# Kernel tuning notes

Hardware: AMD Instinct MI355X
Metric: run time of the kernel (lower is better)

The kernel has to match this reference:

```python
import jax, jax.numpy as jnp
import numpy as np

NAMES = ['tempo', 'chord', 'barbeat', 'type', 'pitch', 'duration', 'velocity']
VOCABS = [56, 135, 18, 4, 87, 18, 25]
EMBS = [128, 256, 64, 32, 512, 128, 128]
B, S, D, H, L, FF = 2, 2048, 512, 8, 8, 2048
HD = D // H
EPS = 1e-6


def _layernorm(x, g, b):
    m = x.mean(-1, keepdims=True)
    v = ((x - m) ** 2).mean(-1, keepdims=True)
    return (x - m) / jnp.sqrt(v + 1e-5) * g + b


def _rope(x, cos, sin):
    x1, x2 = jnp.split(x, 2, -1)
    return x * cos + jnp.concatenate([-x2, x1], -1) * sin


def _causal_linear_attn(q, k, v):
    # kernelized causal linear attention: phi = elu + 1, cumulative-sum normalization
    q = jax.nn.elu(q) + 1.0
    k = jax.nn.elu(k) + 1.0
    kv = jnp.cumsum(jnp.einsum('bshd,bshm->bshdm', k, v), axis=1)  # [B,S,H,HD,HD]
    z = 1.0 / (jnp.einsum('bshd,bshd->bsh', q, jnp.cumsum(k, axis=1)) + EPS)
    return jnp.einsum('bshd,bshdm->bshm', q, kv) * z[..., None]


def _forward(inputs, target, emb_tables, in_W, in_b, Wq, bq, Wk, bk, Wv, bv, Wo, bo,
             ln1_g, ln1_b, ln2_g, ln2_b, W1, b1, W2, b2, norm_g, norm_b, pWs, pbs, catW, catb):
    # multi-field embedding, each scaled by sqrt(d_emb) (CPEmbedding)
    embs = [emb_tables[i][inputs[..., i]] * jnp.sqrt(jnp.float32(EMBS[i])) for i in range(7)]
    x = jnp.concatenate(embs, -1) @ in_W + in_b  # [B,S,D]
    # PositionalEncoding: original indexes pe at position seq_len -> single d_model vector
    div = jnp.exp(jnp.arange(0, D, 2, dtype=jnp.float32) * (-np.log(10000.0) / D))
    pe = jnp.zeros((D,), jnp.float32).at[0::2].set(jnp.sin(S * div)).at[1::2].set(jnp.cos(S * div))
    x = x + pe
    # rotary tables for head_dim
    inv_freq = 1.0 / (10000.0 ** (jnp.arange(0, HD, 2, dtype=jnp.float32) / HD))
    fr = jnp.arange(S, dtype=jnp.float32)[:, None] * inv_freq[None, :]
    ang = jnp.concatenate([fr, fr], -1)  # [S,HD]
    cos = jnp.cos(ang)[None, :, None, :]
    sin = jnp.sin(ang)[None, :, None, :]
    for l in range(L):
        q = (x @ Wq[l] + bq[l]).reshape(B, S, H, HD)
        k = (x @ Wk[l] + bk[l]).reshape(B, S, H, HD)
        v = (x @ Wv[l] + bv[l]).reshape(B, S, H, HD)
        q = _rope(q, cos, sin)
        k = _rope(k, cos, sin)
        a = _causal_linear_attn(q, k, v).reshape(B, S, D) @ Wo[l] + bo[l]
        x = x + a
        y = x = _layernorm(x, ln1_g[l], ln1_b[l])
        y = jax.nn.gelu(y @ W1[l] + b1[l], approximate=False) @ W2[l] + b2[l]
        x = _layernorm(x + y, ln2_g[l], ln2_b[l])
    x = _layernorm(x, norm_g, norm_b)
    # MultiProj with teacher-forced type embedding (target branch)
    emb_t = emb_tables[3][target[..., 3]] * jnp.sqrt(jnp.float32(EMBS[3]))
    proj_type = (x @ pWs[3] + pbs[3]) * jnp.sqrt(jnp.float32(VOCABS[3]))  # from pre-concat x
    xc = jnp.concatenate([x, emb_t], -1) @ catW + catb
    outs = []
    for i in range(7):
        if i == 3:
            outs.append(proj_type)
        else:
            outs.append((xc @ pWs[i] + pbs[i]) * jnp.sqrt(jnp.float32(VOCABS[i])))
    return jnp.concatenate(outs, -1)  # [B,S,sum(VOCABS)=343]


def setup_inputs():
    key = jax.random.key(0)
    kit = iter(jax.random.split(key, 64))
    s = 0.02
    d = {}
    d['inputs'] = jax.random.randint(next(kit), (B, S, 7), 0, 4)
    d['target'] = jax.random.randint(next(kit), (B, S, 7), 0, 4)
    for i, n in enumerate(NAMES):
        d['emb_' + n] = jax.random.normal(next(kit), (VOCABS[i], EMBS[i]), jnp.float32) * s
    E = sum(EMBS)
    d['in_W'] = jax.random.normal(next(kit), (E, D)) * s
    d['in_b'] = jnp.zeros((D,))
    for nm, sh in [('Wq', (L, D, D)), ('Wk', (L, D, D)), ('Wv', (L, D, D)), ('Wo', (L, D, D)), ('W1', (L, D, FF)), ('W2', (L, FF, D))]:
        d[nm] = jax.random.normal(next(kit), sh) * s
    for nm, sh in [('bq', (L, D)), ('bk', (L, D)), ('bv', (L, D)), ('bo', (L, D)), ('b1', (L, FF)), ('b2', (L, D)), ('ln1_b', (L, D)), ('ln2_b', (L, D)), ('norm_b', (D,)), ('catb', (D,))]:
        d[nm] = jnp.zeros(sh)
    d['ln1_g'] = jnp.ones((L, D))
    d['ln2_g'] = jnp.ones((L, D))
    d['norm_g'] = jnp.ones((D,))
    for i, n in enumerate(NAMES):
        d['pW_' + n] = jax.random.normal(next(kit), (D, VOCABS[i])) * s
        d['pb_' + n] = jnp.zeros((VOCABS[i],))
    d['catW'] = jax.random.normal(next(kit), (D + 32, D)) * s
    return d


def reference(inputs, target, emb_tempo, emb_chord, emb_barbeat, emb_type, emb_pitch, emb_duration, emb_velocity,
              in_W, in_b, Wq, bq, Wk, bk, Wv, bv, Wo, bo, ln1_g, ln1_b, ln2_g, ln2_b, W1, b1, W2, b2,
              norm_g, norm_b, pW_tempo, pb_tempo, pW_chord, pb_chord, pW_barbeat, pb_barbeat, pW_type, pb_type,
              pW_pitch, pb_pitch, pW_duration, pb_duration, pW_velocity, pb_velocity, catW, catb):
    emb_tables = [emb_tempo, emb_chord, emb_barbeat, emb_type, emb_pitch, emb_duration, emb_velocity]
    pWs = [pW_tempo, pW_chord, pW_barbeat, pW_type, pW_pitch, pW_duration, pW_velocity]
    pbs = [pb_tempo, pb_chord, pb_barbeat, pb_type, pb_pitch, pb_duration, pb_velocity]
    return _forward(inputs, target, emb_tables, in_W, in_b, Wq, bq, Wk, bk, Wv, bv, Wo, bo,
                    ln1_g, ln1_b, ln2_g, ln2_b, W1, b1, W2, b2, norm_g, norm_b, pWs, pbs, catW, catb)
```

## Files before the change

kernel.cpp:

```cpp
#include <hip/hip_runtime.h>
#include <math.h>

typedef unsigned short u16;
typedef short bf16x8 __attribute__((ext_vector_type(8)));
typedef float f32x4 __attribute__((ext_vector_type(4)));
typedef u16 u16x4 __attribute__((ext_vector_type(4)));
typedef u16 u16x8 __attribute__((ext_vector_type(8)));

#define NB 2
#define NS 2048
#define ND 512
#define NH 8
#define NHD 64
#define NL 8
#define NFF 2048
#define NM (NB*NS)
#define NE 1248
#define NEP 1280
#define NXC 576
#define CHK 64
#define NCH (NS/CHK)
#define QKVW 1536

__device__ inline float b2f(u16 u){ union{ unsigned int i; float f;} x; x.i = ((unsigned int)u)<<16; return x.f; }
__device__ inline u16 f2b(float f){ union{ float f; unsigned int i;} x; x.f=f; unsigned int r = x.i + 0x7fffu + ((x.i>>16)&1u); return (u16)(r>>16); }

__global__ void k_tables(float* rc, float* rs, float* pe){
  int tid = blockIdx.x*blockDim.x + threadIdx.x;
  if (tid < NS*32){
    int s = tid >> 5, j = tid & 31;
    double inv = exp(-(double)(2*j) * log(10000.0) / (double)NHD);
    double ang = (double)s * inv;
    rc[tid] = (float)cos(ang);
    rs[tid] = (float)sin(ang);
  }
  if (tid < ND/2){
    double div = exp(-(double)(2*tid) * log(10000.0) / (double)ND);
    double ang = (double)NS * div;
    pe[2*tid]   = (float)sin(ang);
    pe[2*tid+1] = (float)cos(ang);
  }
}

__global__ void k_embed(const int* __restrict__ inp,
    const float* __restrict__ e0, const float* __restrict__ e1, const float* __restrict__ e2,
    const float* __restrict__ e3, const float* __restrict__ e4, const float* __restrict__ e5,
    const float* __restrict__ e6, u16* __restrict__ xe)
{
  int row = blockIdx.x;
  int i0 = inp[row*7+0], i1 = inp[row*7+1], i2 = inp[row*7+2], i3 = inp[row*7+3],
      i4 = inp[row*7+4], i5 = inp[row*7+5], i6 = inp[row*7+6];
  size_t base = (size_t)row*NEP;
  for (int c = threadIdx.x; c < NEP; c += 256){
    float val = 0.f;
    if      (c < 128)  val = e0[i0*128 + c]        * 11.3137084990f;
    else if (c < 384)  val = e1[i1*256 + (c-128)]  * 16.0f;
    else if (c < 448)  val = e2[i2*64  + (c-384)]  * 8.0f;
    else if (c < 480)  val = e3[i3*32  + (c-448)]  * 5.6568542495f;
    else if (c < 992)  val = e4[i4*512 + (c-480)]  * 22.6274169980f;
    else if (c < 1120) val = e5[i5*128 + (c-992)]  * 11.3137084990f;
    else if (c < NE)   val = e6[i6*128 + (c-1120)] * 11.3137084990f;
    xe[base + c] = f2b(val);
  }
}

__device__ inline void trans_tile(const float* __restrict__ W, u16* __restrict__ WT,
                                  int K, int N, int Kpad, int bx, int by){
  __shared__ float t[32][33];
  int tx = threadIdx.x & 31, ty = threadIdx.x >> 5;
  int k0 = by*32, n0 = bx*32;
  #pragma unroll
  for (int i=0;i<4;i++){
    int k = k0 + ty + i*8, n = n0 + tx;
    t[ty+i*8][tx] = (k<K && n<N) ? W[(size_t)k*N + n] : 0.f;
  }
  __syncthreads();
  #pragma unroll
  for (int i=0;i<4;i++){
    int n = n0 + ty + i*8, k = k0 + tx;
    if (n<N && k<Kpad) WT[(size_t)n*Kpad + k] = f2b(t[tx][ty+i*8]);
  }
}
__global__ void k_trans(const float* __restrict__ W, u16* __restrict__ WT, int K, int N, int Kpad){
  trans_tile(W, WT, K, N, Kpad, blockIdx.x, blockIdx.y);
}
__global__ void k_trans4(const float* __restrict__ Wq, const float* __restrict__ Wk,
                         const float* __restrict__ Wv, const float* __restrict__ Wo,
                         u16* __restrict__ dst){
  int z = blockIdx.z, l = z>>2, s = z&3;
  const float* W = (s==0?Wq:s==1?Wk:s==2?Wv:Wo) + (size_t)l*ND*ND;
  trans_tile(W, dst + (size_t)z*ND*ND, ND, ND, ND, blockIdx.x, blockIdx.y);
}
__global__ void k_transw(const float* __restrict__ W1l, const float* __restrict__ W2l,
                         u16* __restrict__ w1T, u16* __restrict__ w2T){
  int bid = blockIdx.x;
  if (bid < 1024) trans_tile(W1l, w1T, ND, NFF, ND, bid & 63, bid >> 6);
  else { bid -= 1024; trans_tile(W2l, w2T, NFF, ND, NFF, bid & 15, bid >> 4); }
}

template<int ACT, int NT, int TM>
__global__ __launch_bounds__(256) void k_gemm(
    const u16* __restrict__ A, const u16* __restrict__ BT,
    const float* __restrict__ bias, float* __restrict__ Cf, u16* __restrict__ Cb,
    int N, int klen, int lda, int ldb, int ldc,
    int koff, float* __restrict__ Cf2,
    const float* __restrict__ rc, const float* __restrict__ rs)
{
  constexpr int MREP = TM/32;
  __shared__ u16 As[TM*64];
  __shared__ u16 Bs[NT*32*64];
  int tid = threadIdx.x;
  int w = tid >> 6, lane = tid & 63;

  int kz = blockIdx.z;
  A  += (size_t)kz*koff;
  BT += (size_t)kz*koff;
  if (kz){ Cf = Cf2; bias = nullptr; }

  int nwg = gridDim.x*gridDim.y;
  int d = blockIdx.y*gridDim.x + blockIdx.x;
  int wl = ((nwg & 7) == 0) ? ((d & 7)*(nwg >> 3) + (d >> 3)) : d;
  int bx = wl % gridDim.x, by = wl / gridDim.x;
  int m0 = by*TM, n0 = bx*(NT*32);

  f32x4 acc[MREP][NT];
  #pragma unroll
  for (int m=0;m<MREP;m++)
    #pragma unroll
    for (int n=0;n<NT;n++) acc[m][n] = (f32x4){0.f,0.f,0.f,0.f};

  int lg = lane>>3;
  int cg = (lane&7) ^ lg;
  const u16* ag = A  + (size_t)(m0 + w*(TM/4) + lg)*lda + cg*8;
  const u16* bg = BT + (size_t)(n0 + w*(NT*8) + lg)*ldb + cg*8;
  int wr = (w>>1)*(TM/2), wc = (w&1)*(NT*16);
  int lr = lane & 15;
  int rx = lr & 7;
  int cb_ = lane >> 4;
  int g = lane >> 4;

  int nk = klen >> 6;
  for (int t = 0; t < nk; ++t){
    int k0 = t << 6;
    #pragma unroll
    for (int i=0;i<TM/32;i++)
      __builtin_amdgcn_global_load_lds(
        (__attribute__((address_space(1))) void*)(void*)(ag + (size_t)(i*8)*lda + k0),
        (__attribute__((address_space(3))) void*)(&As[(w*(TM/4) + i*8)*64]), 16, 0, 0);
    #pragma unroll
    for (int j=0;j<NT;j++)
      __builtin_amdgcn_global_load_lds(
        (__attribute__((address_space(1))) void*)(void*)(bg + (size_t)(j*8)*ldb + k0),
        (__attribute__((address_space(3))) void*)(&Bs[(w*(NT*8) + j*8)*64]), 16, 0, 0);
    __syncthreads();
    #pragma unroll
    for (int kk=0;kk<2;kk++){
      int gA = ((kk*4 + cb_) ^ rx) * 8;
      bf16x8 af[MREP], bfr[NT];
      #pragma unroll
      for (int m=0;m<MREP;m++) af[m]  = *(const bf16x8*)&As[(wr + m*16 + lr)*64 + gA];
      #pragma unroll
      for (int n=0;n<NT;n++)   bfr[n] = *(const bf16x8*)&Bs[(wc + n*16 + lr)*64 + gA];
      #pragma unroll
      for (int m=0;m<MREP;m++)
        #pragma unroll
        for (int n=0;n<NT;n++)
          acc[m][n] = __builtin_amdgcn_mfma_f32_16x16x32_bf16(af[m], bfr[n], acc[m][n], 0,0,0);
    }
    __syncthreads();
  }

  if (ACT == 2){
    int colb = n0 + wc;
    if (colb < 1024){
      #pragma unroll
      for (int n=0;n<2;n++){
        int j = n*16 + lr;
        float bv1 = bias ? bias[colb+j]    : 0.f;
        float bv2 = bias ? bias[colb+j+32] : 0.f;
        #pragma unroll
        for (int m=0;m<MREP;m++){
          #pragma unroll
          for (int r=0;r<4;r++){
            int row = m0 + wr + m*16 + g*4 + r;
            int s = row & (NS-1);
            float c = rc[s*32+j], sn = rs[s*32+j];
            float a1 = acc[m][n][r]   + bv1;
            float a2 = acc[m][n+2][r] + bv2;
            float r1 = a1*c - a2*sn, r2 = a2*c + a1*sn;
            Cb[(size_t)row*ldc + colb + j]      = f2b((r1 > 0.f) ? r1+1.f : expf(r1));
            Cb[(size_t)row*ldc + colb + j + 32] = f2b((r2 > 0.f) ? r2+1.f : expf(r2));
          }
        }
      }
    } else {
      #pragma unroll
      for (int n=0;n<NT;n++){
        int col = colb + n*16 + lr;
        float bv = bias ? bias[col] : 0.f;
        #pragma unroll
        for (int m=0;m<MREP;m++)
          #pragma unroll
          for (int r=0;r<4;r++){
            int row = m0 + wr + m*16 + g*4 + r;
            Cb[(size_t)row*ldc + col] = f2b(acc[m][n][r] + bv);
          }
      }
    }
    return;
  }

  #pragma unroll
  for (int n=0;n<NT;n++){
    int col = n0 + wc + n*16 + lr;
    if (col < N){
      float bv = bias ? bias[col] : 0.f;
      #pragma unroll
      for (int m=0;m<MREP;m++){
        #pragma unroll
        for (int r=0;r<4;r++){
          int row = m0 + wr + m*16 + g*4 + r;
          float v = acc[m][n][r] + bv;
          if (ACT==1) v = 0.5f*v*(1.f+erff(v*0.70710678118654752f));
          if (Cf) Cf[(size_t)row*ldc + col] = v;
          if (Cb) Cb[(size_t)row*ldc + col] = f2b(v);
        }
      }
    }
  }
}

__global__ __launch_bounds__(256) void k_att1(const u16* __restrict__ qkv, float* __restrict__ pref){
  int c = blockIdx.x, h = blockIdx.y, b = blockIdx.z;
  __shared__ u16 Kt[64*64];
  __shared__ u16 Vt[80*64];
  int tid = threadIdx.x;
  {
    int t = tid & 63, dseg = (tid>>6)*16;
    const u16* kg = qkv + ((size_t)(b*NS + c*CHK + t))*QKVW + 512 + h*NHD + dseg;
    u16x8 k0 = *(const u16x8*)kg;
    u16x8 k1 = *(const u16x8*)(kg+8);
    u16x8 v0 = *(const u16x8*)(kg+512);
    u16x8 v1 = *(const u16x8*)(kg+520);
    #pragma unroll
    for (int e=0;e<8;e++){
      int d0 = dseg+e, d1 = dseg+8+e;
      Kt[(d0*64+t) ^ ((d0&7)<<3)] = k0[e];
      Kt[(d1*64+t) ^ ((d1&7)<<3)] = k1[e];
      Vt[(d0*64+t) ^ ((d0&7)<<3)] = v0[e];
      Vt[(d1*64+t) ^ ((d1&7)<<3)] = v1[e];
    }
    if (tid < 64) Vt[4096 + tid] = 0x3F80;
    for (int e = tid; e < 15*64; e += 256){
      int r = 65 + (e>>6), tt = e&63;
      Vt[(r*64+tt) ^ ((r&7)<<3)] = 0;
    }
  }
  __syncthreads();
  int lane = tid & 63, w = tid >> 6;
  int lr = lane & 15, lk = (lane>>4)*8;
  f32x4 acc[5];
  #pragma unroll
  for (int i=0;i<5;i++) acc[i] = (f32x4){0.f,0.f,0.f,0.f};
  #pragma unroll
  for (int kk=0;kk<2;kk++){
    int mcol = w*16 + lr;
    bf16x8 bfrag = *(const bf16x8*)&Kt[(mcol*64 + kk*32 + lk) ^ ((mcol&7)<<3)];
    #pragma unroll
    for (int fr=0; fr<5; fr++){
      int arow = fr*16 + lr;
      bf16x8 afrag = *(const bf16x8*)&Vt[(arow*64 + kk*32 + lk) ^ ((arow&7)<<3)];
      acc[fr] = __builtin_amdgcn_mfma_f32_16x16x32_bf16(afrag, bfrag, acc[fr], 0,0,0);
    }
  }
  size_t base = (((size_t)(b*NH + h))*NCH + c)*5120;
  int g = lane>>4;
  #pragma unroll
  for (int fr=0; fr<5; fr++)
    #pragma unroll
    for (int r=0;r<4;r++)
      pref[base + (fr*16 + g*4 + r)*64 + w*16 + lr] = acc[fr][r];
}

__global__ __launch_bounds__(256) void k_att2(float* __restrict__ pref){
  int bh = blockIdx.y;
  int e = blockIdx.x*256 + threadIdx.x;
  size_t base = (size_t)bh*NCH*5120 + e;
  float v[NCH];
  #pragma unroll
  for (int c=0;c<NCH;c++) v[c] = pref[base + (size_t)c*5120];
  float run = 0.f;
  #pragma unroll
  for (int c=0;c<NCH;c++){ float t = v[c]; pref[base + (size_t)c*5120] = run; run += t; }
}

__global__ __launch_bounds__(256) void k_att3(const u16* __restrict__ qkv,
    const float* __restrict__ pref, u16* __restrict__ outa)
{
  int c = blockIdx.x, h = blockIdx.y, b = blockIdx.z;
  __shared__ u16 Qs[4096], Ks[4096], Sm[4096];
  __shared__ u16 Vt[5120], Ps[5120];
  __shared__ float dens[64];
  int tid = threadIdx.x;
  {
    int row = tid>>2, seg = (tid&3)*16;
    const u16* qg = qkv + ((size_t)(b*NS + c*CHK + row))*QKVW + h*NHD + seg;
    u16x8 q0 = *(const u16x8*)qg;
    u16x8 q1 = *(const u16x8*)(qg+8);
    u16x8 kk0 = *(const u16x8*)(qg+512);
    u16x8 kk1 = *(const u16x8*)(qg+520);
    int sw = (row&7)<<3;
    *(u16x8*)&Qs[(row*64+seg) ^ sw]     = q0;
    *(u16x8*)&Qs[(row*64+seg+8) ^ sw]   = q1;
    *(u16x8*)&Ks[(row*64+seg) ^ sw]     = kk0;
    *(u16x8*)&Ks[(row*64+seg+8) ^ sw]   = kk1;
  }
  {
    int t = tid&63, dseg = (tid>>6)*16;
    const u16* vg = qkv + ((size_t)(b*NS + c*CHK + t))*QKVW + 1024 + h*NHD + dseg;
    u16x8 v0 = *(const u16x8*)vg;
    u16x8 v1 = *(const u16x8*)(vg+8);
    #pragma unroll
    for (int e=0;e<8;e++){
      int d0=dseg+e, d1=dseg+8+e;
      Vt[(d0*64+t)^((d0&7)<<3)] = v0[e];
      Vt[(d1*64+t)^((d1&7)<<3)] = v1[e];
    }
    if (tid<64) Vt[4096+tid] = 0x3F80;
    for (int e=tid; e<15*64; e+=256){
      int r = 65+(e>>6), tt = e&63;
      Vt[(r*64+tt)^((r&7)<<3)] = 0;
    }
  }
  {
    size_t pb = (((size_t)(b*NH + h))*NCH + c)*5120;
    for (int e=tid; e<5120; e+=256){
      int row = e>>6, m = e&63;
      Ps[(row*64+m)^((row&7)<<3)] = f2b(pref[pb+e]);
    }
  }
  __syncthreads();
  int lane = tid&63, w = tid>>6;
  int lr = lane&15, lk = (lane>>4)*8, g = lane>>4;
  f32x4 sacc[4];
  #pragma unroll
  for (int i=0;i<4;i++) sacc[i] = (f32x4){0.f,0.f,0.f,0.f};
  int iq = w*16 + lr;
  #pragma unroll
  for (int kk=0;kk<2;kk++){
    bf16x8 bq = *(const bf16x8*)&Qs[(iq*64 + kk*32 + lk) ^ ((iq&7)<<3)];
    #pragma unroll
    for (int ft=0; ft<4; ft++){
      int tr = ft*16 + lr;
      bf16x8 ak = *(const bf16x8*)&Ks[(tr*64 + kk*32 + lk) ^ ((tr&7)<<3)];
      sacc[ft] = __builtin_amdgcn_mfma_f32_16x16x32_bf16(ak, bq, sacc[ft], 0,0,0);
    }
  }
  #pragma unroll
  for (int ft=0; ft<4; ft++){
    int t0 = ft*16 + g*4;
    u16x4 pk;
    #pragma unroll
    for (int r=0;r<4;r++) pk[r] = f2b((t0+r <= iq) ? sacc[ft][r] : 0.f);
    *(u16x4*)&Sm[(iq*64 + t0) ^ ((iq&7)<<3)] = pk;
  }
  __syncthreads();
  f32x4 acc[5];
  #pragma unroll
  for (int i=0;i<5;i++) acc[i] = (f32x4){0.f,0.f,0.f,0.f};
  #pragma unroll
  for (int kk=0;kk<2;kk++){
    int sw = (iq&7)<<3;
    bf16x8 as = *(const bf16x8*)&Sm[(iq*64 + kk*32 + lk) ^ sw];
    bf16x8 aq = *(const bf16x8*)&Qs[(iq*64 + kk*32 + lk) ^ sw];
    #pragma unroll
    for (int c5=0;c5<5;c5++){
      int col = c5*16 + lr, sw2 = (col&7)<<3;
      bf16x8 bv = *(const bf16x8*)&Vt[(col*64 + kk*32 + lk) ^ sw2];
      bf16x8 bp = *(const bf16x8*)&Ps[(col*64 + kk*32 + lk) ^ sw2];
      acc[c5] = __builtin_amdgcn_mfma_f32_16x16x32_bf16(as, bv, acc[c5], 0,0,0);
      acc[c5] = __builtin_amdgcn_mfma_f32_16x16x32_bf16(aq, bp, acc[c5], 0,0,0);
    }
  }
  if (lr == 0){
    #pragma unroll
    for (int r=0;r<4;r++) dens[w*16 + g*4 + r] = acc[4][r];
  }
  __syncthreads();
  #pragma unroll
  for (int c5=0;c5<4;c5++){
    #pragma unroll
    for (int r=0;r<4;r++){
      int i = w*16 + g*4 + r;
      float z = 1.f/(dens[i] + 1e-6f);
      outa[((size_t)(b*NS + c*CHK + i))*ND + h*NHD + c5*16 + lr] = f2b(acc[c5][r]*z);
    }
  }
}

__global__ __launch_bounds__(256) void k_ln(const float* __restrict__ xin, const float* __restrict__ res,
    const float* __restrict__ res2, float* __restrict__ outx, u16* __restrict__ outb,
    const float* __restrict__ g, const float* __restrict__ bvec)
{
  int row = blockIdx.x, tid = threadIdx.x;
  size_t base = (size_t)row*ND;
  float v0 = xin[base+tid], v1 = xin[base+tid+256];
  if (res){ v0 += res[base+tid]; v1 += res[base+tid+256]; }
  if (res2){ v0 += res2[base+tid]; v1 += res2[base+tid+256]; }
  float s = v0+v1, ss2 = v0*v0 + v1*v1;
  #pragma unroll
  for (int o = 32; o >= 1; o >>= 1){
    s   += __shfl_down(s, o, 64);
    ss2 += __shfl_down(ss2, o, 64);
  }
  __shared__ float red[8];
  int wv = tid >> 6, ln = tid & 63;
  if (ln == 0){ red[wv] = s; red[4+wv] = ss2; }
  __syncthreads();
  float stot  = red[0]+red[1]+red[2]+red[3];
  float sstot = red[4]+red[5]+red[6]+red[7];
  float mean = stot * (1.0f/ND);
  float var  = sstot * (1.0f/ND) - mean*mean;
  float inv = 1.0f / sqrtf(var + 1e-5f);
  float o0 = (v0-mean)*inv*g[tid]     + bvec[tid];
  float o1 = (v1-mean)*inv*g[tid+256] + bvec[tid+256];
  outx[base+tid] = o0; outx[base+tid+256] = o1;
  if (outb){ outb[base+tid] = f2b(o0); outb[base+tid+256] = f2b(o1); }
}

__global__ void k_xc(const float* __restrict__ x, const int* __restrict__ tgt,
                     const float* __restrict__ embt, u16* __restrict__ xc){
  int row = blockIdx.x;
  int id = tgt[row*7+3];
  size_t base = (size_t)row*NXC;
  for (int c = threadIdx.x; c < NXC; c += 256){
    float v = (c < ND) ? x[(size_t)row*ND + c]
            : (c < 544 ? embt[id*32 + (c-ND)]*5.6568542495f : 0.f);
    xc[base + c] = f2b(v);
  }
}

__global__ void k_pack(const float* p0,const float* p1,const float* p2,const float* p3,
                       const float* p4,const float* p5,const float* p6,
                       const float* q0,const float* q1,const float* q2,const float* q3,
                       const float* q4,const float* q5,const float* q6,
                       u16* __restrict__ pwcT, float* __restrict__ pbc,
                       u16* __restrict__ ptT, float* __restrict__ pbt){
  int idx = blockIdx.x*256 + threadIdx.x;
  const int off[8] = {0,56,191,209,213,300,318,343};
  int col = idx >> 9, k = idx & 511;
  if (col < 384){
    u16 v = 0;
    if (col < 343){
      int f = 0;
      while (col >= off[f+1]) f++;
      int cc = col - off[f];
      int V = off[f+1]-off[f];
      const float* P = (f==0)?p0:(f==1)?p1:(f==2)?p2:(f==3)?p3:(f==4)?p4:(f==5)?p5:p6;
      v = f2b(P[(size_t)k*V + cc] * sqrtf((float)V));
    }
    pwcT[(size_t)col*512 + k] = v;
  }
  if (idx < 64*512){
    int n = idx >> 9;
    ptT[idx] = (n < 4) ? f2b(p3[(size_t)k*4 + n]*2.0f) : (u16)0;
  }
  if (idx < 343){
    int c2 = idx, f = 0;
    while (c2 >= off[f+1]) f++;
    int cc = c2 - off[f]; int V = off[f+1]-off[f];
    const float* Q = (f==0)?q0:(f==1)?q1:(f==2)?q2:(f==3)?q3:(f==4)?q4:(f==5)?q5:q6;
    pbc[idx] = Q[cc]*sqrtf((float)V);
  }
  if (idx < 4) pbt[idx] = q3[idx]*2.0f;
}

__global__ void k_bqkv(const float* __restrict__ bq, const float* __restrict__ bk,
                       const float* __restrict__ bv, float* __restrict__ dst,
                       const float* __restrict__ in_b, const float* __restrict__ pe,
                       float* __restrict__ bias_in){
  int idx = blockIdx.x*256 + threadIdx.x;
  if (idx < NL*QKVW){
    int l = idx / QKVW, c = idx % QKVW;
    float v = (c < 512) ? bq[l*512 + c] : (c < 1024) ? bk[l*512 + c - 512] : bv[l*512 + c - 1024];
    dst[idx] = v;
  }
  if (idx < ND) bias_in[idx] = in_b[idx] + pe[idx];
}

extern "C" void kernel_launch(void* const* d_in, const int* in_sizes, int n_in,
                              void* d_out, int out_size, void* d_ws, size_t ws_size,
                              hipStream_t stream)
{
  const int* inputs = (const int*)d_in[0];
  const int* target = (const int*)d_in[1];
  const float* emb[7];
  for (int i=0;i<7;i++) emb[i] = (const float*)d_in[2+i];
  const float* in_W  = (const float*)d_in[9];
  const float* in_b  = (const float*)d_in[10];
  const float* Wq = (const float*)d_in[11];
  const float* Wk = (const float*)d_in[12];
  const float* Wv = (const float*)d_in[13];
  const float* Wo = (const float*)d_in[14];
  const float* W1 = (const float*)d_in[15];
  const float* W2 = (const float*)d_in[16];
  const float* bq = (const float*)d_in[17];
  const float* bk = (const float*)d_in[18];
  const float* bv = (const float*)d_in[19];
  const float* bo = (const float*)d_in[20];
  const float* b1 = (const float*)d_in[21];
  const float* b2 = (const float*)d_in[22];
  const float* ln1_b = (const float*)d_in[23];
  const float* ln2_b = (const float*)d_in[24];
  const float* norm_b = (const float*)d_in[25];
  const float* catb   = (const float*)d_in[26];
  const float* ln1_g = (const float*)d_in[27];
  const float* ln2_g = (const float*)d_in[28];
  const float* norm_g = (const float*)d_in[29];
  const float* pW[7]; const float* pb[7];
  for (int i=0;i<7;i++){ pW[i]=(const float*)d_in[30+2*i]; pb[i]=(const float*)d_in[31+2*i]; }
  const float* catW = (const float*)d_in[44];
  float* outp = (float*)d_out;

  char* base = (char*)d_ws;
  size_t off = 0;
  auto alloc = [&](size_t bytes)->void*{ void* p = base + off; off += bytes; off = (off + 255) & ~(size_t)255; return p; };

  float* x    = (float*)alloc((size_t)NM*ND*4);
  u16*   xb   = (u16*)  alloc((size_t)NM*ND*2);
  u16*   qkvb = (u16*)  alloc((size_t)NM*QKVW*2);
  float* tb   = (float*)alloc((size_t)NM*ND*4);
  float* tb2  = (float*)alloc((size_t)NM*ND*4);
  u16*   ab   = (u16*)  alloc((size_t)NM*ND*2);
  u16*   hb   = (u16*)  alloc((size_t)NM*NFF*2);
  float* rc   = (float*)alloc((size_t)NS*32*4);
  float* rs   = (float*)alloc((size_t)NS*32*4);
  float* pe   = (float*)alloc(ND*4);
  float* pref = (float*)alloc((size_t)NB*NH*NCH*5120*4);
  u16*  qkvoT = (u16*)  alloc((size_t)NL*4*ND*ND*2);
  u16*  w1T   = (u16*)  alloc((size_t)NFF*ND*2);
  u16*  w2T   = (u16*)  alloc((size_t)ND*NFF*2);
  u16*  inWT  = (u16*)  alloc((size_t)ND*NEP*2);
  u16*  catWT = (u16*)  alloc((size_t)ND*NXC*2);
  u16*  pwcT  = (u16*)  alloc((size_t)384*512*2);
  float* pbc  = (float*)alloc(344*4);
  u16*  ptT   = (u16*)  alloc((size_t)64*512*2);
  float* pbt  = (float*)alloc(4*4);
  float* bqkv = (float*)alloc((size_t)NL*QKVW*4);
  float* bias_in = (float*)alloc(ND*4);
  u16*  xeb = hb;
  u16*  xcb = hb;
  u16*  ocb = hb + (size_t)NM*NXC;

  k_tables<<<256, 256, 0, stream>>>(rc, rs, pe);
  k_trans4<<<dim3(16,16,32), 256, 0, stream>>>(Wq, Wk, Wv, Wo, qkvoT);
  k_trans<<<dim3(16,40), 256, 0, stream>>>(in_W, inWT, NE, ND, NEP);
  k_trans<<<dim3(16,18), 256, 0, stream>>>(catW, catWT, 544, ND, NXC);
  k_pack<<<768, 256, 0, stream>>>(pW[0],pW[1],pW[2],pW[3],pW[4],pW[5],pW[6],
                                  pb[0],pb[1],pb[2],pb[3],pb[4],pb[5],pb[6],
                                  pwcT, pbc, ptT, pbt);
  k_bqkv<<<(NL*QKVW+255)/256, 256, 0, stream>>>(bq, bk, bv, bqkv, in_b, pe, bias_in);

  k_embed<<<NM, 256, 0, stream>>>(inputs, emb[0],emb[1],emb[2],emb[3],emb[4],emb[5],emb[6], xeb);
  k_gemm<0,2,128><<<dim3(8,32,1), 256, 0, stream>>>(xeb, inWT, bias_in, x, xb,
      ND, NEP, NEP, NEP, ND, 0, nullptr, nullptr, nullptr);

  dim3 agrid(NCH, NH, NB);
  for (int l = 0; l < NL; l++){
    k_transw<<<2048, 256, 0, stream>>>(W1 + (size_t)l*ND*NFF, W2 + (size_t)l*NFF*ND, w1T, w2T);
    const u16* woT = qkvoT + (size_t)(l*4+3)*ND*ND;
    k_gemm<2,4,64><<<dim3(12,64,1), 256, 0, stream>>>(xb, qkvoT + (size_t)l*4*ND*ND,
        bqkv + l*QKVW, nullptr, qkvb, QKVW, ND, ND, ND, QKVW, 0, nullptr, rc, rs);
    k_att1<<<agrid, 256, 0, stream>>>(qkvb, pref);
    k_att2<<<dim3(20,16), 256, 0, stream>>>(pref);
    k_att3<<<agrid, 256, 0, stream>>>(qkvb, pref, ab);
    k_gemm<0,2,128><<<dim3(8,32,2), 256, 0, stream>>>(ab, woT, bo + l*ND, tb, nullptr,
        ND, 256, ND, ND, ND, 256, tb2, nullptr, nullptr);
    k_ln<<<NM, 256, 0, stream>>>(x, tb, tb2, x, xb, ln1_g + l*ND, ln1_b + l*ND);
    k_gemm<1,2,128><<<dim3(32,32,1), 256, 0, stream>>>(xb, w1T, b1 + l*NFF, nullptr, hb,
        NFF, ND, ND, ND, NFF, 0, nullptr, nullptr, nullptr);
    k_gemm<0,2,128><<<dim3(8,32,2), 256, 0, stream>>>(hb, w2T, b2 + l*ND, tb, nullptr,
        ND, 1024, NFF, NFF, ND, 1024, tb2, nullptr, nullptr);
    k_ln<<<NM, 256, 0, stream>>>(x, tb, tb2, x, xb, ln2_g + l*ND, ln2_b + l*ND);
  }

  k_ln<<<NM, 256, 0, stream>>>(x, nullptr, nullptr, x, xb, norm_g, norm_b);

  k_xc<<<NM, 256, 0, stream>>>(x, target, emb[3], xcb);
  k_gemm<0,2,128><<<dim3(8,32,1), 256, 0, stream>>>(xcb, catWT, catb, nullptr, ocb,
      ND, NXC, NXC, NXC, ND, 0, nullptr, nullptr, nullptr);
  k_gemm<0,2,128><<<dim3(6,32,1), 256, 0, stream>>>(ocb, pwcT, pbc, outp, nullptr,
      343, ND, ND, ND, 343, 0, nullptr, nullptr, nullptr);
  k_gemm<0,2,128><<<dim3(1,32,1), 256, 0, stream>>>(xb, ptT, pbt, outp + 209, nullptr,
      4, ND, ND, ND, 343, 0, nullptr, nullptr, nullptr);
}
```

Baseline: 888.7 us.

## Shrink GEMM tiles to 64 rows and stage QKV rope epilogue through shared memory

Every GEMM launch now uses a 64-row M tile with twice as many blocks, giving more workgroups to fill the CUs. The QKV GEMM drops to a 64-column N tile, so the fused rotary/ELU epilogue can no longer pair columns inside a thread's registers. It instead writes the biased accumulators to a shared-memory tile (reusing the A/B staging buffers), synchronises, and applies the rotation with coalesced row-wise stores. The smaller tiles give less operand reuse per block and add an extra LDS round trip in the epilogue.

```diff
diff --git a/kernel.cpp b/kernel.cpp
--- a/kernel.cpp
+++ b/kernel.cpp
@@ -107,8 +107,9 @@
     const float* __restrict__ rc, const float* __restrict__ rs)
 {
   constexpr int MREP = TM/32;
-  __shared__ u16 As[TM*64];
-  __shared__ u16 Bs[NT*32*64];
+  __shared__ u16 SH[TM*64 + NT*32*64];
+  u16* As = SH;
+  u16* Bs = SH + TM*64;
   int tid = threadIdx.x;
   int w = tid >> 6, lane = tid & 63;
 
@@ -171,40 +172,36 @@
   }
 
   if (ACT == 2){
-    int colb = n0 + wc;
-    if (colb < 1024){
-      #pragma unroll
-      for (int n=0;n<2;n++){
-        int j = n*16 + lr;
-        float bv1 = bias ? bias[colb+j]    : 0.f;
-        float bv2 = bias ? bias[colb+j+32] : 0.f;
+    float* Cs = (float*)SH;
+    #pragma unroll
+    for (int n=0;n<NT;n++){
+      int col = wc + n*16 + lr;
+      float bv = bias ? bias[n0 + col] : 0.f;
+      #pragma unroll
+      for (int m=0;m<MREP;m++)
         #pragma unroll
-        for (int m=0;m<MREP;m++){
-          #pragma unroll
-          for (int r=0;r<4;r++){
-            int row = m0 + wr + m*16 + g*4 + r;
-            int s = row & (NS-1);
-            float c = rc[s*32+j], sn = rs[s*32+j];
-            float a1 = acc[m][n][r]   + bv1;
-            float a2 = acc[m][n+2][r] + bv2;
-            float r1 = a1*c - a2*sn, r2 = a2*c + a1*sn;
-            Cb[(size_t)row*ldc + colb + j]      = f2b((r1 > 0.f) ? r1+1.f : expf(r1));
-            Cb[(size_t)row*ldc + colb + j + 32] = f2b((r2 > 0.f) ? r2+1.f : expf(r2));
-          }
-        }
+        for (int r=0;r<4;r++)
+          Cs[(wr + m*16 + g*4 + r)*64 + col] = acc[m][n][r] + bv;
+    }
+    __syncthreads();
+    if (n0 < 1024){
+      #pragma unroll
+      for (int i=0;i<8;i++){
+        int p = tid + i*256;
+        int row = p >> 5, j = p & 31;
+        float a1 = Cs[row*64 + j], a2 = Cs[row*64 + j + 32];
+        int s = (m0 + row) & (NS-1);
+        float c = rc[s*32+j], sn = rs[s*32+j];
+        float r1 = a1*c - a2*sn, r2 = a2*c + a1*sn;
+        Cb[(size_t)(m0+row)*ldc + n0 + j]      = f2b((r1 > 0.f) ? r1+1.f : expf(r1));
+        Cb[(size_t)(m0+row)*ldc + n0 + j + 32] = f2b((r2 > 0.f) ? r2+1.f : expf(r2));
       }
     } else {
       #pragma unroll
-      for (int n=0;n<NT;n++){
-        int col = colb + n*16 + lr;
-        float bv = bias ? bias[col] : 0.f;
-        #pragma unroll
-        for (int m=0;m<MREP;m++)
-          #pragma unroll
-          for (int r=0;r<4;r++){
-            int row = m0 + wr + m*16 + g*4 + r;
-            Cb[(size_t)row*ldc + col] = f2b(acc[m][n][r] + bv);
-          }
+      for (int i=0;i<16;i++){
+        int p = tid + i*256;
+        int row = p >> 6, c2 = p & 63;
+        Cb[(size_t)(m0+row)*ldc + n0 + c2] = f2b(Cs[row*64 + c2]);
       }
     }
     return;
@@ -562,24 +559,24 @@
   k_bqkv<<<(NL*QKVW+255)/256, 256, 0, stream>>>(bq, bk, bv, bqkv, in_b, pe, bias_in);
 
   k_embed<<<NM, 256, 0, stream>>>(inputs, emb[0],emb[1],emb[2],emb[3],emb[4],emb[5],emb[6], xeb);
-  k_gemm<0,2,128><<<dim3(8,32,1), 256, 0, stream>>>(xeb, inWT, bias_in, x, xb,
+  k_gemm<0,2,64><<<dim3(8,64,1), 256, 0, stream>>>(xeb, inWT, bias_in, x, xb,
       ND, NEP, NEP, NEP, ND, 0, nullptr, nullptr, nullptr);
 
   dim3 agrid(NCH, NH, NB);
   for (int l = 0; l < NL; l++){
     k_transw<<<2048, 256, 0, stream>>>(W1 + (size_t)l*ND*NFF, W2 + (size_t)l*NFF*ND, w1T, w2T);
     const u16* woT = qkvoT + (size_t)(l*4+3)*ND*ND;
-    k_gemm<2,4,64><<<dim3(12,64,1), 256, 0, stream>>>(xb, qkvoT + (size_t)l*4*ND*ND,
+    k_gemm<2,2,64><<<dim3(24,64,1), 256, 0, stream>>>(xb, qkvoT + (size_t)l*4*ND*ND,
         bqkv + l*QKVW, nullptr, qkvb, QKVW, ND, ND, ND, QKVW, 0, nullptr, rc, rs);
     k_att1<<<agrid, 256, 0, stream>>>(qkvb, pref);
     k_att2<<<dim3(20,16), 256, 0, stream>>>(pref);
     k_att3<<<agrid, 256, 0, stream>>>(qkvb, pref, ab);
-    k_gemm<0,2,128><<<dim3(8,32,2), 256, 0, stream>>>(ab, woT, bo + l*ND, tb, nullptr,
+    k_gemm<0,2,64><<<dim3(8,64,2), 256, 0, stream>>>(ab, woT, bo + l*ND, tb, nullptr,
         ND, 256, ND, ND, ND, 256, tb2, nullptr, nullptr);
     k_ln<<<NM, 256, 0, stream>>>(x, tb, tb2, x, xb, ln1_g + l*ND, ln1_b + l*ND);
-    k_gemm<1,2,128><<<dim3(32,32,1), 256, 0, stream>>>(xb, w1T, b1 + l*NFF, nullptr, hb,
+    k_gemm<1,2,64><<<dim3(32,64,1), 256, 0, stream>>>(xb, w1T, b1 + l*NFF, nullptr, hb,
         NFF, ND, ND, ND, NFF, 0, nullptr, nullptr, nullptr);
-    k_gemm<0,2,128><<<dim3(8,32,2), 256, 0, stream>>>(hb, w2T, b2 + l*ND, tb, nullptr,
+    k_gemm<0,2,64><<<dim3(8,64,2), 256, 0, stream>>>(hb, w2T, b2 + l*ND, tb, nullptr,
         ND, 1024, NFF, NFF, ND, 1024, tb2, nullptr, nullptr);
     k_ln<<<NM, 256, 0, stream>>>(x, tb, tb2, x, xb, ln2_g + l*ND, ln2_b + l*ND);
   }
@@ -587,10 +584,10 @@
   k_ln<<<NM, 256, 0, stream>>>(x, nullptr, nullptr, x, xb, norm_g, norm_b);
 
   k_xc<<<NM, 256, 0, stream>>>(x, target, emb[3], xcb);
-  k_gemm<0,2,128><<<dim3(8,32,1), 256, 0, stream>>>(xcb, catWT, catb, nullptr, ocb,
+  k_gemm<0,2,64><<<dim3(8,64,1), 256, 0, stream>>>(xcb, catWT, catb, nullptr, ocb,
       ND, NXC, NXC, NXC, ND, 0, nullptr, nullptr, nullptr);
-  k_gemm<0,2,128><<<dim3(6,32,1), 256, 0, stream>>>(ocb, pwcT, pbc, outp, nullptr,
+  k_gemm<0,2,64><<<dim3(6,64,1), 256, 0, stream>>>(ocb, pwcT, pbc, outp, nullptr,
       343, ND, ND, ND, 343, 0, nullptr, nullptr, nullptr);
-  k_gemm<0,2,128><<<dim3(1,32,1), 256, 0, stream>>>(xb, ptT, pbt, outp + 209, nullptr,
+  k_gemm<0,2,64><<<dim3(1,64,1), 256, 0, stream>>>(xb, ptT, pbt, outp + 209, nullptr,
       4, ND, ND, ND, 343, 0, nullptr, nullptr, nullptr);
 }
```

Result: faster. 861.9 us (-3.0%).
